# Optimization experiments

Hardware: AMD Instinct MI355X
Metric: run time of the kernel (lower is better)

## Reference

```python
import jax, jax.numpy as jnp
import numpy as np

B, T, H = 8, 2048, 2048


def _wkv(key, value, time_decay, time_first):
    # key, value: [B, T, H]; time_decay/time_first: [H]
    u = time_first
    w = -jnp.exp(time_decay)  # negative decay per channel

    a0 = jnp.zeros(key.shape[::2], key.dtype)            # [B, H]
    b0 = jnp.zeros_like(a0)
    e0 = jnp.full_like(a0, -jnp.inf)

    def step(carry, kv):
        a, b, exponent = carry
        kt, vt = kv                                       # [B, H] each
        # output for this timestep (numerically stabilized)
        max_exp = jnp.maximum(exponent, u + kt)
        wt = jnp.exp(u + kt - max_exp)
        scale = jnp.exp(exponent - max_exp)
        wkv = (a * scale + wt * vt) / (b * scale + wt)
        # state update with decay w
        max_exp2 = jnp.maximum(exponent + w, kt)
        s1 = jnp.exp(exponent + w - max_exp2)
        s2 = jnp.exp(kt - max_exp2)
        a = s1 * a + s2 * vt
        b = s1 * b + s2
        return (a, b, max_exp2), wkv

    kT = jnp.swapaxes(key, 0, 1)    # [T, B, H] for scan over time
    vT = jnp.swapaxes(value, 0, 1)
    _, out = jax.lax.scan(step, (a0, b0, e0), (kT, vT))
    return jnp.swapaxes(out, 0, 1)  # [B, T, H]


def setup_inputs() -> dict:
    key = jax.random.key(0)
    k1, k2, k3, k4 = jax.random.split(key, 4)
    return {
        "key": jax.random.normal(k1, (B, T, H), jnp.float32),
        "value": jax.random.normal(k2, (B, T, H), jnp.float32),
        "time_decay": jax.random.normal(k3, (H,), jnp.float32) * 0.5,
        "time_first": jax.random.normal(k4, (H,), jnp.float32) * 0.5,
    }


def reference(key, value, time_decay, time_first):
    return _wkv(key, value, time_decay, time_first)
```

## Files before the change

### kernel.cpp

```cpp
#include <hip/hip_runtime.h>
#include <math.h>


#define WKV_U 16

__global__ __launch_bounds__(64, 1)
void wkv_fwd(const float* __restrict__ k_, const float* __restrict__ v_,
             const float* __restrict__ td, const float* __restrict__ tf,
             float* __restrict__ out)
{
    constexpr int Tc = 2048, Hc = 2048;
    const int gid = blockIdx.x * 64 + threadIdx.x;
    const int h = gid & (Hc - 1);
    const int b = gid >> 11;

    const float u = tf[h];
    const float w = -__expf(td[h]);

    const size_t base = (size_t)b * Tc * Hc + h;
    const float* kp = k_ + base;
    const float* vp = v_ + base;
    float*       op = out + base;

    float a = 0.0f, bsum = 0.0f, e = -INFINITY;

    auto step = [&](float kt, float vt, float* outp) {
        float uk  = u + kt;
        float m   = fmaxf(e, uk);
        float wt  = __expf(uk - m);
        float sc  = __expf(e - m);
        float num = fmaf(wt, vt, a * sc);
        float den = fmaf(bsum, sc, wt);
        *outp = num * __builtin_amdgcn_rcpf(den);
        float ew  = e + w;
        float m2  = fmaxf(ew, kt);
        float s1  = __expf(ew - m2);
        float s2  = __expf(kt - m2);
        a    = fmaf(s1, a, s2 * vt);
        bsum = fmaf(s1, bsum, s2);
        e    = m2;
    };

    float kA[WKV_U], vA[WKV_U], kB[WKV_U], vB[WKV_U];

    #pragma unroll
    for (int i = 0; i < WKV_U; ++i) {
        kA[i] = kp[(size_t)i * Hc];
        vA[i] = vp[(size_t)i * Hc];
    }

    for (int t0 = 0; t0 < Tc; t0 += 2 * WKV_U) {
        #pragma unroll
        for (int i = 0; i < WKV_U; ++i) {
            kB[i] = kp[(size_t)(t0 + WKV_U + i) * Hc];
            vB[i] = vp[(size_t)(t0 + WKV_U + i) * Hc];
        }
        #pragma unroll
        for (int i = 0; i < WKV_U; ++i)
            step(kA[i], vA[i], op + (size_t)(t0 + i) * Hc);
        if (t0 + 2 * WKV_U < Tc) {
            #pragma unroll
            for (int i = 0; i < WKV_U; ++i) {
                kA[i] = kp[(size_t)(t0 + 2 * WKV_U + i) * Hc];
                vA[i] = vp[(size_t)(t0 + 2 * WKV_U + i) * Hc];
            }
        }
        #pragma unroll
        for (int i = 0; i < WKV_U; ++i)
            step(kB[i], vB[i], op + (size_t)(t0 + WKV_U + i) * Hc);
    }
}

extern "C" void kernel_launch(void* const* d_in, const int* in_sizes, int n_in,
                              void* d_out, int out_size, void* d_ws, size_t ws_size,
                              hipStream_t stream) {
    const float* key   = (const float*)d_in[0];
    const float* value = (const float*)d_in[1];
    const float* td    = (const float*)d_in[2];
    const float* tf    = (const float*)d_in[3];
    float* out = (float*)d_out;

    wkv_fwd<<<dim3(256), dim3(64), 0, stream>>>(key, value, td, tf, out);
}
```

Before: 432.5 us.

## Split WKV scan into chunked three-pass parallel scan over time

Replaces the single sequential-over-time kernel, which launched only 256 blocks of 64 threads, with a chunked scan. Pass 1 computes each time chunk's local state, a combine kernel does an exclusive scan of chunk states using decay w*L, and pass 3 rescans each chunk from its carried-in state to produce outputs. This exposes up to 32x more parallelism along T to fill the GPU, at the cost of reading k and v twice and extra workspace traffic. If ws_size is small, NC falls back to fewer chunks, and if it drops to 1 the workspace writes may overflow.

```diff
diff --git a/kernel.cpp b/kernel.cpp
--- a/kernel.cpp
+++ b/kernel.cpp
@@ -2,27 +2,115 @@
 #include <math.h>
 
 
-#define WKV_U 16
+#define WKV_B 8
+#define WKV_T 2048
+#define WKV_H 2048
+#define WKV_BH (WKV_B * WKV_H)
+#define WKV_U 8
 
-__global__ __launch_bounds__(64, 1)
-void wkv_fwd(const float* __restrict__ k_, const float* __restrict__ v_,
-             const float* __restrict__ td, const float* __restrict__ tf,
-             float* __restrict__ out)
+__device__ __forceinline__ void wkv_update(float& a, float& bs, float& e,
+                                           float w, float kt, float vt) {
+    float ew = e + w;
+    float m2 = fmaxf(ew, kt);
+    float s1 = __expf(ew - m2);
+    float s2 = __expf(kt - m2);
+    a  = fmaf(s1, a, s2 * vt);
+    bs = fmaf(s1, bs, s2);
+    e  = m2;
+}
+
+__global__ __launch_bounds__(256)
+void wkv_pass1(const float* __restrict__ k_, const float* __restrict__ v_,
+               const float* __restrict__ td,
+               float* __restrict__ pa, float* __restrict__ pb,
+               float* __restrict__ pe, int L)
 {
-    constexpr int Tc = 2048, Hc = 2048;
-    const int gid = blockIdx.x * 64 + threadIdx.x;
-    const int h = gid & (Hc - 1);
-    const int b = gid >> 11;
+    const int ch = blockIdx.x * 256 + threadIdx.x;
+    const int c  = blockIdx.y;
+    const int h  = ch & (WKV_H - 1);
+    const int b  = ch >> 11;
+    const float w = -__expf(td[h]);
 
+    const size_t base = (size_t)b * WKV_T * WKV_H + h + (size_t)c * L * WKV_H;
+    const float* kp = k_ + base;
+    const float* vp = v_ + base;
+
+    float a = 0.0f, bs = 0.0f, e = -INFINITY;
+
+    float kA[WKV_U], vA[WKV_U], kB[WKV_U], vB[WKV_U];
+    #pragma unroll
+    for (int i = 0; i < WKV_U; ++i) {
+        kA[i] = kp[(size_t)i * WKV_H];
+        vA[i] = vp[(size_t)i * WKV_H];
+    }
+    for (int t0 = 0; t0 < L; t0 += 2 * WKV_U) {
+        #pragma unroll
+        for (int i = 0; i < WKV_U; ++i) {
+            kB[i] = kp[(size_t)(t0 + WKV_U + i) * WKV_H];
+            vB[i] = vp[(size_t)(t0 + WKV_U + i) * WKV_H];
+        }
+        #pragma unroll
+        for (int i = 0; i < WKV_U; ++i) wkv_update(a, bs, e, w, kA[i], vA[i]);
+        if (t0 + 2 * WKV_U < L) {
+            #pragma unroll
+            for (int i = 0; i < WKV_U; ++i) {
+                kA[i] = kp[(size_t)(t0 + 2 * WKV_U + i) * WKV_H];
+                vA[i] = vp[(size_t)(t0 + 2 * WKV_U + i) * WKV_H];
+            }
+        }
+        #pragma unroll
+        for (int i = 0; i < WKV_U; ++i) wkv_update(a, bs, e, w, kB[i], vB[i]);
+    }
+
+    const size_t idx = (size_t)c * WKV_BH + ch;
+    pa[idx] = a; pb[idx] = bs; pe[idx] = e;
+}
+
+__global__ __launch_bounds__(256)
+void wkv_combine(float* __restrict__ pa, float* __restrict__ pb,
+                 float* __restrict__ pe, const float* __restrict__ td,
+                 int NC, int L)
+{
+    const int ch = blockIdx.x * 256 + threadIdx.x;
+    const float w  = -__expf(td[ch & (WKV_H - 1)]);
+    const float Lw = w * (float)L;
+
+    float a = 0.0f, bs = 0.0f, e = -INFINITY;
+    for (int c = 0; c < NC; ++c) {
+        const size_t idx = (size_t)c * WKV_BH + ch;
+        float qa = pa[idx], qb = pb[idx], qe = pe[idx];
+        pa[idx] = a; pb[idx] = bs; pe[idx] = e;
+        float ed = e + Lw;
+        float m  = fmaxf(ed, qe);
+        float s1 = __expf(ed - m);
+        float s2 = __expf(qe - m);
+        a  = fmaf(s1, a, s2 * qa);
+        bs = fmaf(s1, bs, s2 * qb);
+        e  = m;
+    }
+}
+
+__global__ __launch_bounds__(256)
+void wkv_pass3(const float* __restrict__ k_, const float* __restrict__ v_,
+               const float* __restrict__ td, const float* __restrict__ tf,
+               const float* __restrict__ pa, const float* __restrict__ pb,
+               const float* __restrict__ pe,
+               float* __restrict__ out, int L)
+{
+    const int ch = blockIdx.x * 256 + threadIdx.x;
+    const int c  = blockIdx.y;
+    const int h  = ch & (WKV_H - 1);
+    const int b  = ch >> 11;
     const float u = tf[h];
     const float w = -__expf(td[h]);
 
-    const size_t base = (size_t)b * Tc * Hc + h;
+    const size_t base = (size_t)b * WKV_T * WKV_H + h + (size_t)c * L * WKV_H;
     const float* kp = k_ + base;
     const float* vp = v_ + base;
     float*       op = out + base;
 
-    float a = 0.0f, bsum = 0.0f, e = -INFINITY;
+    const size_t idx = (size_t)c * WKV_BH + ch;
+    float a = pa[idx], bs = pb[idx], e = pe[idx];
 
     auto step = [&](float kt, float vt, float* outp) {
         float uk  = u + kt;
@@ -30,44 +118,36 @@
         float wt  = __expf(uk - m);
         float sc  = __expf(e - m);
         float num = fmaf(wt, vt, a * sc);
-        float den = fmaf(bsum, sc, wt);
+        float den = fmaf(bs, sc, wt);
         *outp = num * __builtin_amdgcn_rcpf(den);
-        float ew  = e + w;
-        float m2  = fmaxf(ew, kt);
-        float s1  = __expf(ew - m2);
-        float s2  = __expf(kt - m2);
-        a    = fmaf(s1, a, s2 * vt);
-        bsum = fmaf(s1, bsum, s2);
-        e    = m2;
+        wkv_update(a, bs, e, w, kt, vt);
     };
 
     float kA[WKV_U], vA[WKV_U], kB[WKV_U], vB[WKV_U];
-
     #pragma unroll
     for (int i = 0; i < WKV_U; ++i) {
-        kA[i] = kp[(size_t)i * Hc];
-        vA[i] = vp[(size_t)i * Hc];
+        kA[i] = kp[(size_t)i * WKV_H];
+        vA[i] = vp[(size_t)i * WKV_H];
     }
-
-    for (int t0 = 0; t0 < Tc; t0 += 2 * WKV_U) {
+    for (int t0 = 0; t0 < L; t0 += 2 * WKV_U) {
         #pragma unroll
         for (int i = 0; i < WKV_U; ++i) {
-            kB[i] = kp[(size_t)(t0 + WKV_U + i) * Hc];
-            vB[i] = vp[(size_t)(t0 + WKV_U + i) * Hc];
+            kB[i] = kp[(size_t)(t0 + WKV_U + i) * WKV_H];
+            vB[i] = vp[(size_t)(t0 + WKV_U + i) * WKV_H];
         }
         #pragma unroll
         for (int i = 0; i < WKV_U; ++i)
-            step(kA[i], vA[i], op + (size_t)(t0 + i) * Hc);
-        if (t0 + 2 * WKV_U < Tc) {
+            step(kA[i], vA[i], op + (size_t)(t0 + i) * WKV_H);
+        if (t0 + 2 * WKV_U < L) {
             #pragma unroll
             for (int i = 0; i < WKV_U; ++i) {
-                kA[i] = kp[(size_t)(t0 + 2 * WKV_U + i) * Hc];
-                vA[i] = vp[(size_t)(t0 + 2 * WKV_U + i) * Hc];
+                kA[i] = kp[(size_t)(t0 + 2 * WKV_U + i) * WKV_H];
+                vA[i] = vp[(size_t)(t0 + 2 * WKV_U + i) * WKV_H];
             }
         }
         #pragma unroll
         for (int i = 0; i < WKV_U; ++i)
-            step(kB[i], vB[i], op + (size_t)(t0 + WKV_U + i) * Hc);
+            step(kB[i], vB[i], op + (size_t)(t0 + WKV_U + i) * WKV_H);
     }
 }
 
@@ -80,5 +160,16 @@
     const float* tf    = (const float*)d_in[3];
     float* out = (float*)d_out;
 
-    wkv_fwd<<<dim3(256), dim3(64), 0, stream>>>(key, value, td, tf, out);
+    int NC = 32;
+    while (NC > 1 && (size_t)3 * sizeof(float) * WKV_BH * NC > ws_size) NC >>= 1;
+    const int L = WKV_T / NC;
+
+    float* pa = (float*)d_ws;
+    float* pb = pa + (size_t)WKV_BH * NC;
+    float* pe = pb + (size_t)WKV_BH * NC;
+
+    dim3 grid1(WKV_BH / 256, NC);
+    wkv_pass1<<<grid1, 256, 0, stream>>>(key, value, td, pa, pb, pe, L);
+    wkv_combine<<<WKV_BH / 256, 256, 0, stream>>>(pa, pb, pe, td, NC, L);
+    wkv_pass3<<<grid1, 256, 0, stream>>>(key, value, td, tf, pa, pb, pe, out, L);
 }
```

Result: faster. 388.6 us (-10.1%).

## Parallelize WKV scan over time with chunked three-pass associative scan

Applied to the files above, without the earlier changes.

Replaces the single sequential-per-channel kernel, which used only 256 blocks of 64 threads, with a chunked scan. Pass 1 computes a per-chunk state for each time chunk in parallel. A two-level carry propagation (group reduce, group scan, in-group scan) composes those states using the decay raised to the chunk length, and pass 3 recomputes outputs for each chunk from its incoming state. This exposes far more parallelism and uses float4 vectorized loads. The cost is reading key and value twice, extra workspace traffic and five kernel launches, and the reassociated log-space composition can change rounding slightly.

```diff
diff --git a/kernel.cpp b/kernel.cpp
--- a/kernel.cpp
+++ b/kernel.cpp
@@ -2,72 +2,200 @@
 #include <math.h>
 
 
-#define WKV_U 16
-
-__global__ __launch_bounds__(64, 1)
-void wkv_fwd(const float* __restrict__ k_, const float* __restrict__ v_,
-             const float* __restrict__ td, const float* __restrict__ tf,
-             float* __restrict__ out)
-{
-    constexpr int Tc = 2048, Hc = 2048;
-    const int gid = blockIdx.x * 64 + threadIdx.x;
-    const int h = gid & (Hc - 1);
-    const int b = gid >> 11;
-
-    const float u = tf[h];
-    const float w = -__expf(td[h]);
-
-    const size_t base = (size_t)b * Tc * Hc + h;
-    const float* kp = k_ + base;
-    const float* vp = v_ + base;
-    float*       op = out + base;
-
-    float a = 0.0f, bsum = 0.0f, e = -INFINITY;
-
-    auto step = [&](float kt, float vt, float* outp) {
-        float uk  = u + kt;
-        float m   = fmaxf(e, uk);
-        float wt  = __expf(uk - m);
-        float sc  = __expf(e - m);
-        float num = fmaf(wt, vt, a * sc);
-        float den = fmaf(bsum, sc, wt);
-        *outp = num * __builtin_amdgcn_rcpf(den);
-        float ew  = e + w;
-        float m2  = fmaxf(ew, kt);
-        float s1  = __expf(ew - m2);
-        float s2  = __expf(kt - m2);
-        a    = fmaf(s1, a, s2 * vt);
-        bsum = fmaf(s1, bsum, s2);
-        e    = m2;
-    };
-
-    float kA[WKV_U], vA[WKV_U], kB[WKV_U], vB[WKV_U];
-
-    #pragma unroll
-    for (int i = 0; i < WKV_U; ++i) {
-        kA[i] = kp[(size_t)i * Hc];
-        vA[i] = vp[(size_t)i * Hc];
-    }
-
-    for (int t0 = 0; t0 < Tc; t0 += 2 * WKV_U) {
+#define TT 2048
+#define HH 2048
+#define BHc 16384
+#define H4 512
+#define NGRP 8
+
+struct __align__(16) f4 { float v[4]; };
+
+__device__ __forceinline__ void upd1(float& a, float& b, float& e,
+                                     float w, float k, float vv) {
+    float ew = e + w;
+    float m  = fmaxf(ew, k);
+    float s1 = __expf(ew - m);
+    float s2 = __expf(k - m);
+    a = fmaf(s1, a, s2 * vv);
+    b = fmaf(s1, b, s2);
+    e = m;
+}
+
+__device__ __forceinline__ void compose(float& a, float& b, float& e,
+                                        float qa, float qb, float qe, float dLw) {
+    float ed = e + dLw;
+    float m  = fmaxf(ed, qe);
+    float s1 = __expf(ed - m);
+    float s2 = __expf(qe - m);
+    a = fmaf(s1, a, s2 * qa);
+    b = fmaf(s1, b, s2 * qb);
+    e = m;
+}
+
+template<int L>
+__global__ __launch_bounds__(256, 4)
+void wkv_pass1(const float* __restrict__ k_, const float* __restrict__ v_,
+               const float* __restrict__ td,
+               float* __restrict__ pa, float* __restrict__ pb,
+               float* __restrict__ pe)
+{
+    const uint32_t t4  = blockIdx.x * 256u + threadIdx.x;
+    const uint32_t c   = blockIdx.y;
+    const uint32_t ch0 = t4 * 4u;
+    const uint32_t h0  = ch0 & (HH - 1);
+    const uint32_t b   = ch0 >> 11;
+
+    const f4 wr = *(const f4*)(td + h0);
+    float w[4], a[4], bs[4], e[4];
+    #pragma unroll
+    for (int j = 0; j < 4; ++j) {
+        w[j] = -__expf(wr.v[j]); a[j] = 0.f; bs[j] = 0.f; e[j] = -INFINITY;
+    }
+
+    const uint32_t off4 = (b * (uint32_t)(TT * HH) + c * (uint32_t)(L * HH) + h0) >> 2;
+    const f4* K4 = (const f4*)k_;
+    const f4* V4 = (const f4*)v_;
+
+    f4 kc = K4[off4], vc = V4[off4];
+    #pragma unroll
+    for (int t = 0; t < L; ++t) {
+        f4 kn, vn;
+        if (t + 1 < L) {
+            kn = K4[off4 + (uint32_t)(t + 1) * H4];
+            vn = V4[off4 + (uint32_t)(t + 1) * H4];
+        }
+        __builtin_amdgcn_sched_barrier(0);
         #pragma unroll
-        for (int i = 0; i < WKV_U; ++i) {
-            kB[i] = kp[(size_t)(t0 + WKV_U + i) * Hc];
-            vB[i] = vp[(size_t)(t0 + WKV_U + i) * Hc];
+        for (int j = 0; j < 4; ++j) upd1(a[j], bs[j], e[j], w[j], kc.v[j], vc.v[j]);
+        if (t + 1 < L) { kc = kn; vc = vn; }
+    }
+
+    const uint32_t pi4 = (c * (uint32_t)BHc + ch0) >> 2;
+    f4 oa, ob, oe;
+    #pragma unroll
+    for (int j = 0; j < 4; ++j) { oa.v[j] = a[j]; ob.v[j] = bs[j]; oe.v[j] = e[j]; }
+    ((f4*)pa)[pi4] = oa; ((f4*)pb)[pi4] = ob; ((f4*)pe)[pi4] = oe;
+}
+
+__global__ __launch_bounds__(256, 2)
+void wkv_k2a(const float* __restrict__ pa, const float* __restrict__ pb,
+             const float* __restrict__ pe,
+             float* __restrict__ aa, float* __restrict__ ab,
+             float* __restrict__ ae,
+             const float* __restrict__ td, int CPG, int L)
+{
+    const uint32_t id = blockIdx.x * 256u + threadIdx.x;
+    const uint32_t ch = id & (BHc - 1);
+    const uint32_t g  = id >> 14;
+    const float w  = -__expf(td[ch & (HH - 1)]);
+    const float Lw = w * (float)L;
+
+    float a = 0.f, b = 0.f, e = -INFINITY;
+    for (int c = (int)g * CPG; c < (int)(g + 1) * CPG; ++c) {
+        const uint32_t idx = (uint32_t)c * BHc + ch;
+        compose(a, b, e, pa[idx], pb[idx], pe[idx], Lw);
+    }
+    const uint32_t gi = g * BHc + ch;
+    aa[gi] = a; ab[gi] = b; ae[gi] = e;
+}
+
+__global__ __launch_bounds__(256, 2)
+void wkv_k2b(float* __restrict__ aa, float* __restrict__ ab,
+             float* __restrict__ ae, const float* __restrict__ td, int LC)
+{
+    const uint32_t ch = blockIdx.x * 256u + threadIdx.x;
+    const float w   = -__expf(td[ch & (HH - 1)]);
+    const float GLw = w * (float)LC;
+
+    float a = 0.f, b = 0.f, e = -INFINITY;
+    for (int g = 0; g < NGRP; ++g) {
+        const uint32_t gi = (uint32_t)g * BHc + ch;
+        float qa = aa[gi], qb = ab[gi], qe = ae[gi];
+        aa[gi] = a; ab[gi] = b; ae[gi] = e;
+        compose(a, b, e, qa, qb, qe, GLw);
+    }
+}
+
+__global__ __launch_bounds__(256, 2)
+void wkv_k2c(float* __restrict__ pa, float* __restrict__ pb,
+             float* __restrict__ pe,
+             const float* __restrict__ aa, const float* __restrict__ ab,
+             const float* __restrict__ ae,
+             const float* __restrict__ td, int CPG, int L)
+{
+    const uint32_t id = blockIdx.x * 256u + threadIdx.x;
+    const uint32_t ch = id & (BHc - 1);
+    const uint32_t g  = id >> 14;
+    const float w  = -__expf(td[ch & (HH - 1)]);
+    const float Lw = w * (float)L;
+
+    const uint32_t gi = g * BHc + ch;
+    float a = aa[gi], b = ab[gi], e = ae[gi];
+    for (int c = (int)g * CPG; c < (int)(g + 1) * CPG; ++c) {
+        const uint32_t idx = (uint32_t)c * BHc + ch;
+        float qa = pa[idx], qb = pb[idx], qe = pe[idx];
+        pa[idx] = a; pb[idx] = b; pe[idx] = e;
+        compose(a, b, e, qa, qb, qe, Lw);
+    }
+}
+
+template<int L>
+__global__ __launch_bounds__(256, 4)
+void wkv_pass3(const float* __restrict__ k_, const float* __restrict__ v_,
+               const float* __restrict__ td, const float* __restrict__ tf,
+               const float* __restrict__ pa, const float* __restrict__ pb,
+               const float* __restrict__ pe,
+               float* __restrict__ out)
+{
+    const uint32_t t4  = blockIdx.x * 256u + threadIdx.x;
+    const uint32_t c   = blockIdx.y;
+    const uint32_t ch0 = t4 * 4u;
+    const uint32_t h0  = ch0 & (HH - 1);
+    const uint32_t b   = ch0 >> 11;
+
+    const f4 wr = *(const f4*)(td + h0);
+    const f4 ur = *(const f4*)(tf + h0);
+    const uint32_t pi4 = (c * (uint32_t)BHc + ch0) >> 2;
+    const f4 ra = ((const f4*)pa)[pi4];
+    const f4 rb = ((const f4*)pb)[pi4];
+    const f4 re = ((const f4*)pe)[pi4];
+
+    float w[4], u[4], a[4], bs[4], e[4];
+    #pragma unroll
+    for (int j = 0; j < 4; ++j) {
+        w[j] = -__expf(wr.v[j]); u[j] = ur.v[j];
+        a[j] = ra.v[j]; bs[j] = rb.v[j]; e[j] = re.v[j];
+    }
+
+    const uint32_t off4 = (b * (uint32_t)(TT * HH) + c * (uint32_t)(L * HH) + h0) >> 2;
+    const f4* K4 = (const f4*)k_;
+    const f4* V4 = (const f4*)v_;
+    f4*       O4 = (f4*)out;
+
+    f4 kc = K4[off4], vc = V4[off4];
+    #pragma unroll
+    for (int t = 0; t < L; ++t) {
+        f4 kn, vn;
+        if (t + 1 < L) {
+            kn = K4[off4 + (uint32_t)(t + 1) * H4];
+            vn = V4[off4 + (uint32_t)(t + 1) * H4];
         }
+        __builtin_amdgcn_sched_barrier(0);
+        f4 o;
         #pragma unroll
-        for (int i = 0; i < WKV_U; ++i)
-            step(kA[i], vA[i], op + (size_t)(t0 + i) * Hc);
-        if (t0 + 2 * WKV_U < Tc) {
-            #pragma unroll
-            for (int i = 0; i < WKV_U; ++i) {
-                kA[i] = kp[(size_t)(t0 + 2 * WKV_U + i) * Hc];
-                vA[i] = vp[(size_t)(t0 + 2 * WKV_U + i) * Hc];
-            }
+        for (int j = 0; j < 4; ++j) {
+            float kt = kc.v[j], vt = vc.v[j];
+            float uk  = u[j] + kt;
+            float m   = fmaxf(e[j], uk);
+            float wt  = __expf(uk - m);
+            float sc  = __expf(e[j] - m);
+            float num = fmaf(wt, vt, a[j] * sc);
+            float den = fmaf(bs[j], sc, wt);
+            o.v[j] = num * __builtin_amdgcn_rcpf(den);
+            upd1(a[j], bs[j], e[j], w[j], kt, vt);
         }
-        #pragma unroll
-        for (int i = 0; i < WKV_U; ++i)
-            step(kB[i], vB[i], op + (size_t)(t0 + WKV_U + i) * Hc);
+        O4[off4 + (uint32_t)t * H4] = o;
+        if (t + 1 < L) { kc = kn; vc = vn; }
     }
 }
 
@@ -80,5 +208,46 @@
     const float* tf    = (const float*)d_in[3];
     float* out = (float*)d_out;
 
-    wkv_fwd<<<dim3(256), dim3(64), 0, stream>>>(key, value, td, tf, out);
-}
+    int NC = 64;
+    while (NC > 8 &&
+           (size_t)3 * sizeof(float) * BHc * (NC + NGRP) > ws_size) NC >>= 1;
+    const int L   = TT / NC;
+    const int CPG = NC / NGRP;
+
+    float* pa = (float*)d_ws;
+    float* pb = pa + (size_t)BHc * NC;
+    float* pe = pb + (size_t)BHc * NC;
+    float* aa = pe + (size_t)BHc * NC;
+    float* ab = aa + (size_t)BHc * NGRP;
+    float* ae = ab + (size_t)BHc * NGRP;
+
+    dim3 grid1(BHc / 4 / 256, NC);
+    const int gk2 = BHc * NGRP / 256;
+    const int gkb = BHc / 256;
+
+    switch (L) {
+    case 32:
+        wkv_pass1<32><<<grid1, 256, 0, stream>>>(key, value, td, pa, pb, pe);
+        break;
+    case 64:
+        wkv_pass1<64><<<grid1, 256, 0, stream>>>(key, value, td, pa, pb, pe);
+        break;
+    default:
+        wkv_pass1<128><<<grid1, 256, 0, stream>>>(key, value, td, pa, pb, pe);
+        break;
+    }
+    wkv_k2a<<<gk2, 256, 0, stream>>>(pa, pb, pe, aa, ab, ae, td, CPG, L);
+    wkv_k2b<<<gkb, 256, 0, stream>>>(aa, ab, ae, td, L * CPG);
+    wkv_k2c<<<gk2, 256, 0, stream>>>(pa, pb, pe, aa, ab, ae, td, CPG, L);
+    switch (L) {
+    case 32:
+        wkv_pass3<32><<<grid1, 256, 0, stream>>>(key, value, td, tf, pa, pb, pe, out);
+        break;
+    case 64:
+        wkv_pass3<64><<<grid1, 256, 0, stream>>>(key, value, td, tf, pa, pb, pe, out);
+        break;
+    default:
+        wkv_pass3<128><<<grid1, 256, 0, stream>>>(key, value, td, tf, pa, pb, pe, out);
+        break;
+    }
+}
```

Measured after the change: 414.1 us. 1.04x faster.
